# Kernel optimization log

Measured on AMD Instinct MI355X. Metric: run time of the kernel, lower is better.

Reference implementation:

```python
import jax, jax.numpy as jnp
import numpy as np

T, B, F_IN = 1024, 256, 87


def _lstm(x, Wih, Whh, b):
    """PyTorch-convention LSTM over seq-first x [T,B,In]; gate order i,f,g,o."""
    H = Whh.shape[1]
    Bz = x.shape[1]

    def step(carry, xt):
        h, c = carry
        z = xt @ Wih.T + h @ Whh.T + b  # [B, 4H]
        i, f, g, o = jnp.split(z, 4, axis=-1)
        c = jax.nn.sigmoid(f) * c + jax.nn.sigmoid(i) * jnp.tanh(g)
        h = jax.nn.sigmoid(o) * jnp.tanh(c)
        return (h, c), h

    init = (jnp.zeros((Bz, H), x.dtype), jnp.zeros((Bz, H), x.dtype))
    _, ys = jax.lax.scan(step, init, x)
    return ys  # [T, B, H]


def setup_inputs() -> dict:
    key = jax.random.key(0)
    ks = jax.random.split(key, 24)

    def p(k, shape, fan):
        s = 1.0 / np.sqrt(fan)
        return jax.random.uniform(k, shape, jnp.float32, -s, s)

    d = {}
    d["x"] = jax.random.normal(ks[0], (T, B, F_IN), jnp.float32)
    # LSTM params (bias = b_ih + b_hh combined; forward-equivalent)
    dims = [(F_IN, 256), (256, 128), (128, 64), (64, 32)]
    ki = 1
    for li, (din, h) in enumerate(dims, start=1):
        d[f"w{li}i"] = p(ks[ki], (4 * h, din), h); ki += 1
        d[f"w{li}h"] = p(ks[ki], (4 * h, h), h); ki += 1
        d[f"b{li}"] = p(ks[ki], (4 * h,), h); ki += 1
    fcs = [(32, 128), (128, 64), (64, 32), (32, 3)]
    for fi, (din, dout) in enumerate(fcs, start=1):
        d[f"f{fi}w"] = p(ks[ki], (dout, din), din); ki += 1
        d[f"f{fi}b"] = p(ks[ki], (dout,), din); ki += 1
    return d


def reference(x, w1i, w1h, b1, w2i, w2h, b2, w3i, w3h, b3, w4i, w4h, b4,
              f1w, f1b, f2w, f2b, f3w, f3b, f4w, f4b):
    h = jnp.tanh(_lstm(x, w1i, w1h, b1))
    h = jnp.tanh(_lstm(h, w2i, w2h, b2))
    h = jnp.tanh(_lstm(h, w3i, w3h, b3))
    h = jnp.tanh(_lstm(h, w4i, w4h, b4)[0])  # [0] -> first timestep, [B,32]
    h = jax.nn.relu(h @ f1w.T + f1b)
    h = jax.nn.relu(h @ f2w.T + f2b)
    h = jax.nn.relu(h @ f3w.T + f3b)
    return h @ f4w.T + f4b  # [B, 3]
```

## Files before the change

kernel.cpp:

```cpp
#include <hip/hip_runtime.h>
#include <math.h>


#define O_W1T 0
#define O_W2T 66816
#define O_W3T 165120
#define O_W4T 189696
#define O_F1T 195840
#define O_F2T 199936
#define O_F3T 208128
#define O_B1  210176
#define O_B2  210944
#define O_B3  211328
#define O_B4  211520
#define O_FLG 211616
#define O_H1  211744
#define O_H2  277280

__global__ __launch_bounds__(256) void prep_kernel(
    const float* __restrict__ w1i, const float* __restrict__ w2i,
    const float* __restrict__ w3i, const float* __restrict__ w4i,
    const float* __restrict__ b1,  const float* __restrict__ b2,
    const float* __restrict__ b3,  const float* __restrict__ b4,
    const float* __restrict__ f1w, const float* __restrict__ f2w,
    const float* __restrict__ f3w, float* __restrict__ ws)
{
    int i = blockIdx.x * 256 + threadIdx.x;
    if (i < 128) ((int*)ws)[O_FLG + i] = 0;
    if (i < 89088) {
        int row = i / 87, k = i - row * 87;
        int g = row >> 8;
        if (g != 1) {
            int base = (g == 0) ? 0 : (g == 2) ? 256 : 512;
            ws[O_W1T + k * 768 + base + (row & 255)] = w1i[i];
        }
    } else if (i < 220160) {
        int l = i - 89088;
        int row = l >> 8, k = l & 255;
        int g = row >> 7;
        if (g != 1) {
            int base = (g == 0) ? 0 : (g == 2) ? 128 : 256;
            ws[O_W2T + k * 384 + base + (row & 127)] = w2i[l];
        }
    } else if (i < 252928) {
        int l = i - 220160;
        int row = l >> 7, k = l & 127;
        int g = row >> 6;
        if (g != 1) {
            int base = (g == 0) ? 0 : (g == 2) ? 64 : 128;
            ws[O_W3T + k * 192 + base + (row & 63)] = w3i[l];
        }
    } else if (i < 261120) {
        int l = i - 252928;
        int row = l >> 6, k = l & 63;
        int g = row >> 5;
        if (g != 1) {
            int base = (g == 0) ? 0 : (g == 2) ? 32 : 64;
            ws[O_W4T + k * 96 + base + (row & 31)] = w4i[l];
        }
    } else if (i < 262144) {
        int l = i - 261120;
        int g = l >> 8;
        if (g != 1) {
            int base = (g == 0) ? 0 : (g == 2) ? 256 : 512;
            ws[O_B1 + base + (l & 255)] = b1[l];
        }
    } else if (i < 262656) {
        int l = i - 262144;
        int g = l >> 7;
        if (g != 1) {
            int base = (g == 0) ? 0 : (g == 2) ? 128 : 256;
            ws[O_B2 + base + (l & 127)] = b2[l];
        }
    } else if (i < 262912) {
        int l = i - 262656;
        int g = l >> 6;
        if (g != 1) {
            int base = (g == 0) ? 0 : (g == 2) ? 64 : 128;
            ws[O_B3 + base + (l & 63)] = b3[l];
        }
    } else if (i < 263040) {
        int l = i - 262912;
        int g = l >> 5;
        if (g != 1) {
            int base = (g == 0) ? 0 : (g == 2) ? 32 : 64;
            ws[O_B4 + base + (l & 31)] = b4[l];
        }
    } else if (i < 267136) {
        int l = i - 263040;
        int j = l >> 5, k = l & 31;
        ws[O_F1T + k * 128 + j] = f1w[l];
    } else if (i < 275328) {
        int l = i - 267136;
        int j = l >> 7, k = l & 127;
        ws[O_F2T + k * 64 + j] = f2w[l];
    } else if (i < 277376) {
        int l = i - 275328;
        int j = l >> 6, k = l & 63;
        ws[O_F3T + k * 32 + j] = f3w[l];
    }
}

__device__ __forceinline__ float frcp(float x) { return __builtin_amdgcn_rcpf(x); }
__device__ __forceinline__ float sigm(float x) { return frcp(1.0f + __expf(-x)); }
__device__ __forceinline__ float tanh_f(float x) { return 1.0f - 2.0f * frcp(1.0f + __expf(2.0f * x)); }
__device__ __forceinline__ float cell(float zi, float zg, float zo) {
    float c = sigm(zi) * tanh_f(zg);
    return tanh_f(sigm(zo) * tanh_f(c));
}

#define FMA4(z, xv, wv) \
    z.x = fmaf(xv, wv.x, z.x); z.y = fmaf(xv, wv.y, z.y); \
    z.z = fmaf(xv, wv.z, z.z); z.w = fmaf(xv, wv.w, z.w);

__global__ __launch_bounds__(512) void lstm_fused_sliced(
    const float* __restrict__ x, float* __restrict__ ws,
    const float* __restrict__ f1b, const float* __restrict__ f2b,
    const float* __restrict__ f3b, const float* __restrict__ f4w,
    const float* __restrict__ f4b, float* __restrict__ out)
{
    const int t = threadIdx.x;
    const int g = blockIdx.x >> 2;
    const int s = blockIdx.x & 3;
    const int row = blockIdx.x;

    __shared__ __align__(16) float xs4[348];
    __shared__ __align__(16) float buf[1536];
    __shared__ __align__(16) float hbuf[1024];
    __shared__ float h3s[64], h4s[32], a1s[128], a2s[64], a3s[32];

    const float* W1T = ws + O_W1T;
    const float* W2T = ws + O_W2T;
    const float* W3T = ws + O_W3T;
    const float* W4T = ws + O_W4T;
    const float* F1T = ws + O_F1T;
    const float* F2T = ws + O_F2T;
    const float* F3T = ws + O_F3T;
    int* flg1 = (int*)ws + O_FLG + g;
    int* flg2 = (int*)ws + O_FLG + 64 + g;

    if (t < 348) xs4[t] = x[g * 348 + t];

    float b1i = 0.f, b1g = 0.f, b1o = 0.f;
    float b2i = 0.f, b2g = 0.f, b2o = 0.f;
    float b3i = 0.f, b3g = 0.f, b3o = 0.f;
    float b4i = 0.f, b4g = 0.f, b4o = 0.f;
    float vf1 = 0.f, vf2 = 0.f, vf3 = 0.f;
    {
        const float* B1p = ws + O_B1;
        const float* B2p = ws + O_B2;
        const float* B3p = ws + O_B3;
        const float* B4p = ws + O_B4;
        int j6 = t & 63, j5 = t & 31;
        if (t < 256) { b1i = B1p[s*64+j6]; b1g = B1p[256+s*64+j6]; b1o = B1p[512+s*64+j6]; }
        if (t < 128) { b2i = B2p[s*32+j5]; b2g = B2p[128+s*32+j5]; b2o = B2p[256+s*32+j5]; vf1 = f1b[t]; }
        if (t < 64)  { b3i = B3p[t]; b3g = B3p[64+t]; b3o = B3p[128+t]; vf2 = f2b[t]; }
        if (t < 32)  { b4i = B4p[t]; b4g = B4p[32+t]; b4o = B4p[64+t]; vf3 = f3b[t]; }
    }
    __syncthreads();

    if (t < 384) {
        const int kk = t / 192;
        const int u  = t - kk * 192;
        const int r  = u / 48;
        const int v  = u - r * 48;
        const int gate = v >> 4, q = v & 15;
        const int col = gate * 256 + s * 64 + q * 4;
        const float* wp = W1T + col;
        const float* xr = xs4 + r * 87;
        const int k0 = kk ? 44 : 0, k1 = kk ? 87 : 44;
        float4 z = {0.f, 0.f, 0.f, 0.f};
        #pragma unroll 4
        for (int k = k0; k < k1; ++k) {
            const float4 wv = *(const float4*)(wp + k * 768);
            const float xv = xr[k];
            FMA4(z, xv, wv);
        }
        *(float4*)&buf[kk * 768 + r * 192 + gate * 64 + q * 4] = z;
    }
    __syncthreads();
    if (t < 256) {
        const int r = t >> 6, j = t & 63;
        const float zi = buf[r*192 + j]       + buf[768 + r*192 + j]       + b1i;
        const float zg = buf[r*192 + 64 + j]  + buf[768 + r*192 + 64 + j]  + b1g;
        const float zo = buf[r*192 + 128 + j] + buf[768 + r*192 + 128 + j] + b1o;
        const float h = cell(zi, zg, zo);
        __hip_atomic_store(&ws[O_H1 + (4*g + r) * 256 + s * 64 + j], h,
                           __ATOMIC_RELAXED, __HIP_MEMORY_SCOPE_AGENT);
    }
    __syncthreads();
    if (t == 0)
        __hip_atomic_fetch_add(flg1, 1, __ATOMIC_RELEASE, __HIP_MEMORY_SCOPE_AGENT);

    if (t == 0) {
        while (__hip_atomic_load(flg1, __ATOMIC_RELAXED, __HIP_MEMORY_SCOPE_AGENT) < 4)
            __builtin_amdgcn_s_sleep(2);
        (void)__hip_atomic_load(flg1, __ATOMIC_ACQUIRE, __HIP_MEMORY_SCOPE_AGENT);
    }
    __syncthreads();
    for (int i = t; i < 1024; i += 512)
        hbuf[i] = __hip_atomic_load(&ws[O_H1 + g * 1024 + i],
                                    __ATOMIC_RELAXED, __HIP_MEMORY_SCOPE_AGENT);
    __syncthreads();

    if (t < 384) {
        const int kk = t / 96;
        const int u  = t - kk * 96;
        const int r  = u / 24;
        const int v  = u - r * 24;
        const int gate = v >> 3, q = v & 7;
        const int col = gate * 128 + s * 32 + q * 4;
        const float* wp = W2T + col;
        const float* hr = hbuf + r * 256;
        const int k0 = kk * 64;
        float4 z = {0.f, 0.f, 0.f, 0.f};
        #pragma unroll 4
        for (int k = k0; k < k0 + 64; ++k) {
            const float4 wv = *(const float4*)(wp + k * 384);
            const float hv = hr[k];
            FMA4(z, hv, wv);
        }
        *(float4*)&buf[kk * 384 + r * 96 + gate * 32 + q * 4] = z;
    }
    __syncthreads();
    if (t < 128) {
        const int r = t >> 5, j = t & 31;
        float zi = b2i, zg = b2g, zo = b2o;
        #pragma unroll
        for (int kk = 0; kk < 4; ++kk) {
            zi += buf[kk*384 + r*96 + j];
            zg += buf[kk*384 + r*96 + 32 + j];
            zo += buf[kk*384 + r*96 + 64 + j];
        }
        const float h = cell(zi, zg, zo);
        __hip_atomic_store(&ws[O_H2 + (4*g + r) * 128 + s * 32 + j], h,
                           __ATOMIC_RELAXED, __HIP_MEMORY_SCOPE_AGENT);
    }
    __syncthreads();
    if (t == 0)
        __hip_atomic_fetch_add(flg2, 1, __ATOMIC_RELEASE, __HIP_MEMORY_SCOPE_AGENT);

    if (t == 0) {
        while (__hip_atomic_load(flg2, __ATOMIC_RELAXED, __HIP_MEMORY_SCOPE_AGENT) < 4)
            __builtin_amdgcn_s_sleep(2);
        (void)__hip_atomic_load(flg2, __ATOMIC_ACQUIRE, __HIP_MEMORY_SCOPE_AGENT);
    }
    __syncthreads();
    if (t < 128)
        hbuf[t] = __hip_atomic_load(&ws[O_H2 + row * 128 + t],
                                    __ATOMIC_RELAXED, __HIP_MEMORY_SCOPE_AGENT);
    __syncthreads();

    if (t < 384) {
        const int kk = t / 48, Q = t - kk * 48;
        const float* wp = W3T + 4 * Q;
        const int k0 = kk * 16;
        float4 z = {0.f, 0.f, 0.f, 0.f};
        #pragma unroll
        for (int k = k0; k < k0 + 16; ++k) {
            const float4 wv = *(const float4*)(wp + k * 192);
            const float hv = hbuf[k];
            FMA4(z, hv, wv);
        }
        *(float4*)&buf[kk * 192 + 4 * Q] = z;
    }
    __syncthreads();
    if (t < 64) {
        float zi = b3i, zg = b3g, zo = b3o;
        #pragma unroll
        for (int kk = 0; kk < 8; ++kk) {
            zi += buf[kk*192 + t];
            zg += buf[kk*192 + 64 + t];
            zo += buf[kk*192 + 128 + t];
        }
        h3s[t] = cell(zi, zg, zo);
    }
    __syncthreads();

    if (t < 384) {
        const int kk = t / 24, Q = t - kk * 24;
        const float* wp = W4T + 4 * Q;
        const int k0 = kk * 4;
        float4 z = {0.f, 0.f, 0.f, 0.f};
        #pragma unroll
        for (int k = k0; k < k0 + 4; ++k) {
            const float4 wv = *(const float4*)(wp + k * 96);
            const float hv = h3s[k];
            FMA4(z, hv, wv);
        }
        *(float4*)&buf[kk * 96 + 4 * Q] = z;
    }
    __syncthreads();
    if (t < 32) {
        float zi = b4i, zg = b4g, zo = b4o;
        #pragma unroll
        for (int kk = 0; kk < 16; ++kk) {
            zi += buf[kk*96 + t];
            zg += buf[kk*96 + 32 + t];
            zo += buf[kk*96 + 64 + t];
        }
        h4s[t] = cell(zi, zg, zo);
    }
    __syncthreads();

    if (t < 256) {
        const int kk = t >> 5, Q = t & 31;
        const float* wp = F1T + 4 * Q;
        const int k0 = kk * 4;
        float4 z = {0.f, 0.f, 0.f, 0.f};
        #pragma unroll
        for (int k = k0; k < k0 + 4; ++k) {
            const float4 wv = *(const float4*)(wp + k * 128);
            const float hv = h4s[k];
            FMA4(z, hv, wv);
        }
        *(float4*)&buf[kk * 128 + 4 * Q] = z;
    }
    __syncthreads();
    if (t < 128) {
        float a = vf1;
        #pragma unroll
        for (int kk = 0; kk < 8; ++kk) a += buf[kk*128 + t];
        a1s[t] = fmaxf(a, 0.0f);
    }
    __syncthreads();

    if (t < 256) {
        const int kk = t >> 4, Q = t & 15;
        const float* wp = F2T + 4 * Q;
        const int k0 = kk * 8;
        float4 z = {0.f, 0.f, 0.f, 0.f};
        #pragma unroll
        for (int k = k0; k < k0 + 8; ++k) {
            const float4 wv = *(const float4*)(wp + k * 64);
            const float hv = a1s[k];
            FMA4(z, hv, wv);
        }
        *(float4*)&buf[kk * 64 + 4 * Q] = z;
    }
    __syncthreads();
    if (t < 64) {
        float a = vf2;
        #pragma unroll
        for (int kk = 0; kk < 16; ++kk) a += buf[kk*64 + t];
        a2s[t] = fmaxf(a, 0.0f);
    }
    __syncthreads();

    if (t < 128) {
        const int kk = t >> 3, Q = t & 7;
        const float* wp = F3T + 4 * Q;
        const int k0 = kk * 4;
        float4 z = {0.f, 0.f, 0.f, 0.f};
        #pragma unroll
        for (int k = k0; k < k0 + 4; ++k) {
            const float4 wv = *(const float4*)(wp + k * 32);
            const float hv = a2s[k];
            FMA4(z, hv, wv);
        }
        *(float4*)&buf[kk * 32 + 4 * Q] = z;
    }
    __syncthreads();
    if (t < 32) {
        float a = vf3;
        #pragma unroll
        for (int kk = 0; kk < 16; ++kk) a += buf[kk*32 + t];
        a3s[t] = fmaxf(a, 0.0f);
    }
    __syncthreads();

    if (t < 3) {
        const float4* wr = (const float4*)(f4w + t * 32);
        float a0 = f4b[t], a1 = 0.f;
        #pragma unroll
        for (int i = 0; i < 8; ++i) {
            const float4 wv = wr[i];
            const float4 hv = *(const float4*)&a3s[4 * i];
            a0 = fmaf(hv.x, wv.x, a0);
            a1 = fmaf(hv.y, wv.y, a1);
            a0 = fmaf(hv.z, wv.z, a0);
            a1 = fmaf(hv.w, wv.w, a1);
        }
        out[row * 3 + t] = a0 + a1;
    }
}

extern "C" void kernel_launch(void* const* d_in, const int* in_sizes, int n_in,
                              void* d_out, int out_size, void* d_ws, size_t ws_size,
                              hipStream_t stream) {
    const float* x   = (const float*)d_in[0];
    const float* w1i = (const float*)d_in[1];
    const float* b1  = (const float*)d_in[3];
    const float* w2i = (const float*)d_in[4];
    const float* b2  = (const float*)d_in[6];
    const float* w3i = (const float*)d_in[7];
    const float* b3  = (const float*)d_in[9];
    const float* w4i = (const float*)d_in[10];
    const float* b4  = (const float*)d_in[12];
    const float* f1w = (const float*)d_in[13];
    const float* f1b = (const float*)d_in[14];
    const float* f2w = (const float*)d_in[15];
    const float* f2b = (const float*)d_in[16];
    const float* f3w = (const float*)d_in[17];
    const float* f3b = (const float*)d_in[18];
    const float* f4w = (const float*)d_in[19];
    const float* f4b = (const float*)d_in[20];
    float* ws  = (float*)d_ws;
    float* out = (float*)d_out;

    prep_kernel<<<1084, 256, 0, stream>>>(w1i, w2i, w3i, w4i, b1, b2, b3, b4,
                                          f1w, f2w, f3w, ws);
    lstm_fused_sliced<<<256, 512, 0, stream>>>(x, ws, f1b, f2b, f3b, f4w, f4b,
                                               out);
}
```

Baseline: 178.9 us.

## Compute one batch row per block and drop inter-block flag synchronization

Each block now computes the whole network for a single batch row, instead of four blocks splitting the hidden units of a four-row group. This removes the global-memory hidden-state exchange, the atomic flag counters and the spin-waits between blocks, along with the flag reset in the prep kernel. In exchange, every block reads the full layer-1 and layer-2 weight matrices rather than a quarter slice, so per-block weight traffic and L2 pressure go up. Unroll factors on the first two matvec loops are also raised.

```diff
diff --git a/kernel.cpp b/kernel.cpp
--- a/kernel.cpp
+++ b/kernel.cpp
@@ -13,9 +13,6 @@
 #define O_B2  210944
 #define O_B3  211328
 #define O_B4  211520
-#define O_FLG 211616
-#define O_H1  211744
-#define O_H2  277280
 
 __global__ __launch_bounds__(256) void prep_kernel(
     const float* __restrict__ w1i, const float* __restrict__ w2i,
@@ -26,7 +23,6 @@
     const float* __restrict__ f3w, float* __restrict__ ws)
 {
     int i = blockIdx.x * 256 + threadIdx.x;
-    if (i < 128) ((int*)ws)[O_FLG + i] = 0;
     if (i < 89088) {
         int row = i / 87, k = i - row * 87;
         int g = row >> 8;
@@ -113,21 +109,19 @@
     z.x = fmaf(xv, wv.x, z.x); z.y = fmaf(xv, wv.y, z.y); \
     z.z = fmaf(xv, wv.z, z.z); z.w = fmaf(xv, wv.w, z.w);
 
-__global__ __launch_bounds__(512) void lstm_fused_sliced(
-    const float* __restrict__ x, float* __restrict__ ws,
+__global__ __launch_bounds__(512) void lstm_fused(
+    const float* __restrict__ x, const float* __restrict__ ws,
     const float* __restrict__ f1b, const float* __restrict__ f2b,
     const float* __restrict__ f3b, const float* __restrict__ f4w,
     const float* __restrict__ f4b, float* __restrict__ out)
 {
     const int t = threadIdx.x;
-    const int g = blockIdx.x >> 2;
-    const int s = blockIdx.x & 3;
-    const int row = blockIdx.x;
-
-    __shared__ __align__(16) float xs4[348];
-    __shared__ __align__(16) float buf[1536];
-    __shared__ __align__(16) float hbuf[1024];
-    __shared__ float h3s[64], h4s[32], a1s[128], a2s[64], a3s[32];
+    const int r = blockIdx.x;
+
+    __shared__ float xs[87];
+    __shared__ float h1[256], h2[128], h3[64], h4[32];
+    __shared__ float a1[128], a2[64], a3[32];
+    __shared__ __align__(16) float ps[1536];
 
     const float* W1T = ws + O_W1T;
     const float* W2T = ws + O_W2T;
@@ -136,252 +130,195 @@
     const float* F1T = ws + O_F1T;
     const float* F2T = ws + O_F2T;
     const float* F3T = ws + O_F3T;
-    int* flg1 = (int*)ws + O_FLG + g;
-    int* flg2 = (int*)ws + O_FLG + 64 + g;
-
-    if (t < 348) xs4[t] = x[g * 348 + t];
 
     float b1i = 0.f, b1g = 0.f, b1o = 0.f;
-    float b2i = 0.f, b2g = 0.f, b2o = 0.f;
-    float b3i = 0.f, b3g = 0.f, b3o = 0.f;
-    float b4i = 0.f, b4g = 0.f, b4o = 0.f;
-    float vf1 = 0.f, vf2 = 0.f, vf3 = 0.f;
+    float b2i = 0.f, b2g = 0.f, b2o = 0.f, vf1 = 0.f;
+    float b3i = 0.f, b3g = 0.f, b3o = 0.f, vf2 = 0.f;
+    float b4i = 0.f, b4g = 0.f, b4o = 0.f, vf3 = 0.f;
     {
         const float* B1p = ws + O_B1;
         const float* B2p = ws + O_B2;
         const float* B3p = ws + O_B3;
         const float* B4p = ws + O_B4;
-        int j6 = t & 63, j5 = t & 31;
-        if (t < 256) { b1i = B1p[s*64+j6]; b1g = B1p[256+s*64+j6]; b1o = B1p[512+s*64+j6]; }
-        if (t < 128) { b2i = B2p[s*32+j5]; b2g = B2p[128+s*32+j5]; b2o = B2p[256+s*32+j5]; vf1 = f1b[t]; }
-        if (t < 64)  { b3i = B3p[t]; b3g = B3p[64+t]; b3o = B3p[128+t]; vf2 = f2b[t]; }
-        if (t < 32)  { b4i = B4p[t]; b4g = B4p[32+t]; b4o = B4p[64+t]; vf3 = f3b[t]; }
-    }
+        if (t < 256) { b1i = B1p[t]; b1g = B1p[256 + t]; b1o = B1p[512 + t]; }
+        if (t < 128) { b2i = B2p[t]; b2g = B2p[128 + t]; b2o = B2p[256 + t]; vf1 = f1b[t]; }
+        if (t < 64)  { b3i = B3p[t]; b3g = B3p[64 + t];  b3o = B3p[128 + t]; vf2 = f2b[t]; }
+        if (t < 32)  { b4i = B4p[t]; b4g = B4p[32 + t];  b4o = B4p[64 + t];  vf3 = f3b[t]; }
+    }
+
+    if (t < 87) xs[t] = x[r * 87 + t];
     __syncthreads();
 
     if (t < 384) {
-        const int kk = t / 192;
-        const int u  = t - kk * 192;
-        const int r  = u / 48;
-        const int v  = u - r * 48;
-        const int gate = v >> 4, q = v & 15;
-        const int col = gate * 256 + s * 64 + q * 4;
-        const float* wp = W1T + col;
-        const float* xr = xs4 + r * 87;
-        const int k0 = kk ? 44 : 0, k1 = kk ? 87 : 44;
-        float4 z = {0.f, 0.f, 0.f, 0.f};
-        #pragma unroll 4
+        const int kp = t / 192, Q = t - kp * 192;
+        const float* wp = W1T + 4 * Q;
+        const int k0 = kp ? 44 : 0, k1 = kp ? 87 : 44;
+        float4 z = {0.f, 0.f, 0.f, 0.f};
+        #pragma unroll 8
         for (int k = k0; k < k1; ++k) {
             const float4 wv = *(const float4*)(wp + k * 768);
-            const float xv = xr[k];
-            FMA4(z, xv, wv);
-        }
-        *(float4*)&buf[kk * 768 + r * 192 + gate * 64 + q * 4] = z;
-    }
-    __syncthreads();
-    if (t < 256) {
-        const int r = t >> 6, j = t & 63;
-        const float zi = buf[r*192 + j]       + buf[768 + r*192 + j]       + b1i;
-        const float zg = buf[r*192 + 64 + j]  + buf[768 + r*192 + 64 + j]  + b1g;
-        const float zo = buf[r*192 + 128 + j] + buf[768 + r*192 + 128 + j] + b1o;
-        const float h = cell(zi, zg, zo);
-        __hip_atomic_store(&ws[O_H1 + (4*g + r) * 256 + s * 64 + j], h,
-                           __ATOMIC_RELAXED, __HIP_MEMORY_SCOPE_AGENT);
-    }
-    __syncthreads();
-    if (t == 0)
-        __hip_atomic_fetch_add(flg1, 1, __ATOMIC_RELEASE, __HIP_MEMORY_SCOPE_AGENT);
-
-    if (t == 0) {
-        while (__hip_atomic_load(flg1, __ATOMIC_RELAXED, __HIP_MEMORY_SCOPE_AGENT) < 4)
-            __builtin_amdgcn_s_sleep(2);
-        (void)__hip_atomic_load(flg1, __ATOMIC_ACQUIRE, __HIP_MEMORY_SCOPE_AGENT);
-    }
-    __syncthreads();
-    for (int i = t; i < 1024; i += 512)
-        hbuf[i] = __hip_atomic_load(&ws[O_H1 + g * 1024 + i],
-                                    __ATOMIC_RELAXED, __HIP_MEMORY_SCOPE_AGENT);
+            FMA4(z, xs[k], wv);
+        }
+        *(float4*)&ps[kp * 768 + 4 * Q] = z;
+    }
+    __syncthreads();
+    if (t < 256)
+        h1[t] = cell(ps[t] + ps[768 + t] + b1i,
+                     ps[256 + t] + ps[1024 + t] + b1g,
+                     ps[512 + t] + ps[1280 + t] + b1o);
     __syncthreads();
 
     if (t < 384) {
-        const int kk = t / 96;
-        const int u  = t - kk * 96;
-        const int r  = u / 24;
-        const int v  = u - r * 24;
-        const int gate = v >> 3, q = v & 7;
-        const int col = gate * 128 + s * 32 + q * 4;
-        const float* wp = W2T + col;
-        const float* hr = hbuf + r * 256;
-        const int k0 = kk * 64;
-        float4 z = {0.f, 0.f, 0.f, 0.f};
-        #pragma unroll 4
+        const int kp = t / 96, Q = t - kp * 96;
+        const float* wp = W2T + 4 * Q;
+        const int k0 = kp * 64;
+        float4 z = {0.f, 0.f, 0.f, 0.f};
+        #pragma unroll 8
         for (int k = k0; k < k0 + 64; ++k) {
             const float4 wv = *(const float4*)(wp + k * 384);
-            const float hv = hr[k];
-            FMA4(z, hv, wv);
-        }
-        *(float4*)&buf[kk * 384 + r * 96 + gate * 32 + q * 4] = z;
+            FMA4(z, h1[k], wv);
+        }
+        *(float4*)&ps[kp * 384 + 4 * Q] = z;
     }
     __syncthreads();
     if (t < 128) {
-        const int r = t >> 5, j = t & 31;
         float zi = b2i, zg = b2g, zo = b2o;
         #pragma unroll
-        for (int kk = 0; kk < 4; ++kk) {
-            zi += buf[kk*384 + r*96 + j];
-            zg += buf[kk*384 + r*96 + 32 + j];
-            zo += buf[kk*384 + r*96 + 64 + j];
-        }
-        const float h = cell(zi, zg, zo);
-        __hip_atomic_store(&ws[O_H2 + (4*g + r) * 128 + s * 32 + j], h,
-                           __ATOMIC_RELAXED, __HIP_MEMORY_SCOPE_AGENT);
-    }
-    __syncthreads();
-    if (t == 0)
-        __hip_atomic_fetch_add(flg2, 1, __ATOMIC_RELEASE, __HIP_MEMORY_SCOPE_AGENT);
-
-    if (t == 0) {
-        while (__hip_atomic_load(flg2, __ATOMIC_RELAXED, __HIP_MEMORY_SCOPE_AGENT) < 4)
-            __builtin_amdgcn_s_sleep(2);
-        (void)__hip_atomic_load(flg2, __ATOMIC_ACQUIRE, __HIP_MEMORY_SCOPE_AGENT);
-    }
-    __syncthreads();
-    if (t < 128)
-        hbuf[t] = __hip_atomic_load(&ws[O_H2 + row * 128 + t],
-                                    __ATOMIC_RELAXED, __HIP_MEMORY_SCOPE_AGENT);
+        for (int kp = 0; kp < 4; ++kp) {
+            zi += ps[kp * 384 + t];
+            zg += ps[kp * 384 + 128 + t];
+            zo += ps[kp * 384 + 256 + t];
+        }
+        h2[t] = cell(zi, zg, zo);
+    }
     __syncthreads();
 
     if (t < 384) {
-        const int kk = t / 48, Q = t - kk * 48;
+        const int kp = t / 48, Q = t - kp * 48;
         const float* wp = W3T + 4 * Q;
-        const int k0 = kk * 16;
+        const int k0 = kp * 16;
         float4 z = {0.f, 0.f, 0.f, 0.f};
         #pragma unroll
         for (int k = k0; k < k0 + 16; ++k) {
             const float4 wv = *(const float4*)(wp + k * 192);
-            const float hv = hbuf[k];
-            FMA4(z, hv, wv);
-        }
-        *(float4*)&buf[kk * 192 + 4 * Q] = z;
+            FMA4(z, h2[k], wv);
+        }
+        *(float4*)&ps[kp * 192 + 4 * Q] = z;
     }
     __syncthreads();
     if (t < 64) {
         float zi = b3i, zg = b3g, zo = b3o;
         #pragma unroll
-        for (int kk = 0; kk < 8; ++kk) {
-            zi += buf[kk*192 + t];
-            zg += buf[kk*192 + 64 + t];
-            zo += buf[kk*192 + 128 + t];
-        }
-        h3s[t] = cell(zi, zg, zo);
+        for (int kp = 0; kp < 8; ++kp) {
+            zi += ps[kp * 192 + t];
+            zg += ps[kp * 192 + 64 + t];
+            zo += ps[kp * 192 + 128 + t];
+        }
+        h3[t] = cell(zi, zg, zo);
     }
     __syncthreads();
 
     if (t < 384) {
-        const int kk = t / 24, Q = t - kk * 24;
+        const int kp = t / 24, Q = t - kp * 24;
         const float* wp = W4T + 4 * Q;
-        const int k0 = kk * 4;
+        const int k0 = kp * 4;
         float4 z = {0.f, 0.f, 0.f, 0.f};
         #pragma unroll
         for (int k = k0; k < k0 + 4; ++k) {
             const float4 wv = *(const float4*)(wp + k * 96);
-            const float hv = h3s[k];
-            FMA4(z, hv, wv);
-        }
-        *(float4*)&buf[kk * 96 + 4 * Q] = z;
+            FMA4(z, h3[k], wv);
+        }
+        *(float4*)&ps[kp * 96 + 4 * Q] = z;
     }
     __syncthreads();
     if (t < 32) {
         float zi = b4i, zg = b4g, zo = b4o;
         #pragma unroll
-        for (int kk = 0; kk < 16; ++kk) {
-            zi += buf[kk*96 + t];
-            zg += buf[kk*96 + 32 + t];
-            zo += buf[kk*96 + 64 + t];
-        }
-        h4s[t] = cell(zi, zg, zo);
+        for (int kp = 0; kp < 16; ++kp) {
+            zi += ps[kp * 96 + t];
+            zg += ps[kp * 96 + 32 + t];
+            zo += ps[kp * 96 + 64 + t];
+        }
+        h4[t] = cell(zi, zg, zo);
     }
     __syncthreads();
 
     if (t < 256) {
-        const int kk = t >> 5, Q = t & 31;
+        const int kp = t >> 5, Q = t & 31;
         const float* wp = F1T + 4 * Q;
-        const int k0 = kk * 4;
+        const int k0 = kp * 4;
         float4 z = {0.f, 0.f, 0.f, 0.f};
         #pragma unroll
         for (int k = k0; k < k0 + 4; ++k) {
             const float4 wv = *(const float4*)(wp + k * 128);
-            const float hv = h4s[k];
-            FMA4(z, hv, wv);
-        }
-        *(float4*)&buf[kk * 128 + 4 * Q] = z;
+            FMA4(z, h4[k], wv);
+        }
+        *(float4*)&ps[kp * 128 + 4 * Q] = z;
     }
     __syncthreads();
     if (t < 128) {
         float a = vf1;
         #pragma unroll
-        for (int kk = 0; kk < 8; ++kk) a += buf[kk*128 + t];
-        a1s[t] = fmaxf(a, 0.0f);
+        for (int kp = 0; kp < 8; ++kp) a += ps[kp * 128 + t];
+        a1[t] = fmaxf(a, 0.0f);
     }
     __syncthreads();
 
     if (t < 256) {
-        const int kk = t >> 4, Q = t & 15;
+        const int kp = t >> 4, Q = t & 15;
         const float* wp = F2T + 4 * Q;
-        const int k0 = kk * 8;
+        const int k0 = kp * 8;
         float4 z = {0.f, 0.f, 0.f, 0.f};
         #pragma unroll
         for (int k = k0; k < k0 + 8; ++k) {
             const float4 wv = *(const float4*)(wp + k * 64);
-            const float hv = a1s[k];
-            FMA4(z, hv, wv);
-        }
-        *(float4*)&buf[kk * 64 + 4 * Q] = z;
+            FMA4(z, a1[k], wv);
+        }
+        *(float4*)&ps[kp * 64 + 4 * Q] = z;
     }
     __syncthreads();
     if (t < 64) {
         float a = vf2;
         #pragma unroll
-        for (int kk = 0; kk < 16; ++kk) a += buf[kk*64 + t];
-        a2s[t] = fmaxf(a, 0.0f);
+        for (int kp = 0; kp < 16; ++kp) a += ps[kp * 64 + t];
+        a2[t] = fmaxf(a, 0.0f);
     }
     __syncthreads();
 
     if (t < 128) {
-        const int kk = t >> 3, Q = t & 7;
+        const int kp = t >> 3, Q = t & 7;
         const float* wp = F3T + 4 * Q;
-        const int k0 = kk * 4;
+        const int k0 = kp * 4;
         float4 z = {0.f, 0.f, 0.f, 0.f};
         #pragma unroll
         for (int k = k0; k < k0 + 4; ++k) {
             const float4 wv = *(const float4*)(wp + k * 32);
-            const float hv = a2s[k];
-            FMA4(z, hv, wv);
-        }
-        *(float4*)&buf[kk * 32 + 4 * Q] = z;
+            FMA4(z, a2[k], wv);
+        }
+        *(float4*)&ps[kp * 32 + 4 * Q] = z;
     }
     __syncthreads();
     if (t < 32) {
         float a = vf3;
         #pragma unroll
-        for (int kk = 0; kk < 16; ++kk) a += buf[kk*32 + t];
-        a3s[t] = fmaxf(a, 0.0f);
+        for (int kp = 0; kp < 16; ++kp) a += ps[kp * 32 + t];
+        a3[t] = fmaxf(a, 0.0f);
     }
     __syncthreads();
 
     if (t < 3) {
         const float4* wr = (const float4*)(f4w + t * 32);
-        float a0 = f4b[t], a1 = 0.f;
+        float a0 = f4b[t], a1v = 0.f;
         #pragma unroll
         for (int i = 0; i < 8; ++i) {
             const float4 wv = wr[i];
-            const float4 hv = *(const float4*)&a3s[4 * i];
+            const float4 hv = *(const float4*)&a3[4 * i];
             a0 = fmaf(hv.x, wv.x, a0);
-            a1 = fmaf(hv.y, wv.y, a1);
+            a1v = fmaf(hv.y, wv.y, a1v);
             a0 = fmaf(hv.z, wv.z, a0);
-            a1 = fmaf(hv.w, wv.w, a1);
-        }
-        out[row * 3 + t] = a0 + a1;
+            a1v = fmaf(hv.w, wv.w, a1v);
+        }
+        out[r * 3 + t] = a0 + a1v;
     }
 }
 
@@ -410,6 +347,5 @@
 
     prep_kernel<<<1084, 256, 0, stream>>>(w1i, w2i, w3i, w4i, b1, b2, b3, b4,
                                           f1w, f2w, f3w, ws);
-    lstm_fused_sliced<<<256, 512, 0, stream>>>(x, ws, f1b, f2b, f3b, f4w, f4b,
-                                               out);
+    lstm_fused<<<256, 512, 0, stream>>>(x, ws, f1b, f2b, f3b, f4w, f4b, out);
 }
```

New measurement: 166.6 us. 1.07x faster.
